# Kernel optimization log

Hardware: AMD Instinct MI355X
Metric: run time of the kernel (lower is better)

Reference implementation:

```python
import jax, jax.numpy as jnp
import numpy as np

N = 50000       # nodes
E = 800000      # edges (before self-loops)
F_IN = 128      # per-head input features (nfeat * t_size, t_size=1)
NHID = 128
NHEADS = 4
NCLASS = 64
NEG_SLOPE = 0.2   # GATConv leakyrelu negative_slope
ALPHA = 0.2       # outer LeakyReLU(alpha)


def setup_inputs():
    key = jax.random.key(0)
    ks = jax.random.split(key, 10)
    type_emb = jax.random.normal(ks[0], (NHEADS, N, F_IN), jnp.float32)
    edge = jax.random.randint(ks[1], (2, E), 0, N, dtype=jnp.int32)
    W = jax.random.normal(ks[2], (NHEADS, F_IN, NHID), jnp.float32) / np.sqrt(F_IN).astype(np.float32)
    att_src = jax.random.normal(ks[3], (NHEADS, NHID), jnp.float32) * 0.1
    att_dst = jax.random.normal(ks[4], (NHEADS, NHID), jnp.float32) * 0.1
    bias = jnp.zeros((NHEADS, NHID), jnp.float32)
    W_out = jax.random.normal(ks[5], (NHID * NHEADS, NCLASS), jnp.float32) / np.sqrt(NHID * NHEADS).astype(np.float32)
    att_src_out = jax.random.normal(ks[6], (NCLASS,), jnp.float32) * 0.1
    att_dst_out = jax.random.normal(ks[7], (NCLASS,), jnp.float32) * 0.1
    bias_out = jnp.zeros((NCLASS,), jnp.float32)
    return {"type_emb": type_emb, "edge": edge, "W": W, "att_src": att_src,
            "att_dst": att_dst, "bias": bias, "W_out": W_out,
            "att_src_out": att_src_out, "att_dst_out": att_dst_out,
            "bias_out": bias_out}


def _gat_conv(x, src, dst, W, a_src, a_dst, b):
    """PyG GATConv, heads=1, with self-loops already in (src, dst)."""
    xs = x @ W                                      # [N, H]
    e = jax.nn.leaky_relu((xs @ a_src)[src] + (xs @ a_dst)[dst], NEG_SLOPE)  # [E']
    # segment softmax over destination nodes (every node has a self-loop -> no empty segment)
    m = jax.ops.segment_max(e, dst, num_segments=N)
    ex = jnp.exp(e - m[dst])
    denom = jax.ops.segment_sum(ex, dst, num_segments=N)
    alpha = ex / denom[dst]                          # [E']
    out = jax.ops.segment_sum(alpha[:, None] * xs[src], dst, num_segments=N)  # [N, H]
    return out + b


def reference(type_emb, edge, W, att_src, att_dst, bias, W_out,
              att_src_out, att_dst_out, bias_out):
    loop = jnp.arange(N, dtype=edge.dtype)
    src = jnp.concatenate([edge[0], loop])
    dst = jnp.concatenate([edge[1], loop])
    # per-head GraphAttentionLayer: GATConv -> LeakyReLU(alpha) (dropout inactive)
    heads = [jax.nn.leaky_relu(
                 _gat_conv(type_emb[i], src, dst, W[i], att_src[i], att_dst[i], bias[i]),
                 ALPHA)
             for i in range(NHEADS)]
    x = jnp.concatenate(heads, axis=1)               # [N, NHID*NHEADS]
    y = jax.nn.leaky_relu(
            _gat_conv(x, src, dst, W_out, att_src_out, att_dst_out, bias_out),
            ALPHA)
    return jnp.tanh(y)                               # [N, NCLASS]
```

## Files before the change

kernel.cpp:

```cpp
#include <hip/hip_runtime.h>
#include <cmath>

#define NN 50000
#define EE 800000
#define ETOT (EE + NN)
#define NSCAN ((NN + 1023) / 1024)

typedef __bf16 v8bf __attribute__((ext_vector_type(8)));
typedef float f32x4 __attribute__((ext_vector_type(4)));

__device__ __forceinline__ float lrelu(float x){ return x > 0.0f ? x : 0.2f * x; }
__device__ __forceinline__ int bcast_i(int v, int j){ return __builtin_amdgcn_readlane(v, j); }
__device__ __forceinline__ float bcast_f(float v, int j){
  return __uint_as_float(__builtin_amdgcn_readlane(__float_as_uint(v), j));
}
__device__ __forceinline__ unsigned short f2bf_rne(float x){
  unsigned int u = __float_as_uint(x);
  u += 0x7fffu + ((u >> 16) & 1u);
  return (unsigned short)(u >> 16);
}
__device__ __forceinline__ float bf2f(unsigned short b){
  return __uint_as_float(((unsigned int)b) << 16);
}

__global__ void k_hist(const int* __restrict__ dst, int* __restrict__ cnt){
  int i = blockIdx.x * 256 + threadIdx.x;
  if (i >= ETOT) return;
  int d = (i < EE) ? dst[i] : (i - EE);
  atomicAdd(&cnt[d], 1);
}

__global__ void k_scan1(const int* __restrict__ cnt, int* __restrict__ part){
  __shared__ int sm[256];
  int b = blockIdx.x, t = threadIdx.x;
  int base = b * 1024 + t * 4;
  int s = 0;
  #pragma unroll
  for (int j = 0; j < 4; j++) if (base + j < NN) s += cnt[base + j];
  sm[t] = s; __syncthreads();
  for (int off = 128; off; off >>= 1){
    if (t < off) sm[t] += sm[t + off];
    __syncthreads();
  }
  if (t == 0) part[b] = sm[0];
}

__global__ void k_scan2(const int* __restrict__ part, int* __restrict__ part2){
  if (threadIdx.x == 0 && blockIdx.x == 0){
    int run = 0;
    for (int i = 0; i < NSCAN; i++){ part2[i] = run; run += part[i]; }
  }
}

__global__ void k_scan3(const int* __restrict__ cnt, const int* __restrict__ part2,
                        int* __restrict__ rowptr){
  __shared__ int sm[256];
  int b = blockIdx.x, t = threadIdx.x;
  int base = b * 1024 + t * 4;
  int v[4]; int s = 0;
  #pragma unroll
  for (int j = 0; j < 4; j++){ v[j] = (base + j < NN) ? cnt[base + j] : 0; s += v[j]; }
  sm[t] = s; __syncthreads();
  for (int off = 1; off < 256; off <<= 1){
    int x = (t >= off) ? sm[t - off] : 0;
    __syncthreads();
    sm[t] += x;
    __syncthreads();
  }
  int run = part2[b] + sm[t] - s;
  #pragma unroll
  for (int j = 0; j < 4; j++){
    if (base + j < NN){ rowptr[base + j] = run; run += v[j]; }
  }
  if (b == 0 && t == 0) rowptr[NN] = ETOT;
}

__global__ void k_scatter(const int* __restrict__ src, const int* __restrict__ dst,
                          const int* __restrict__ rowptr, int* __restrict__ fill,
                          int* __restrict__ csr){
  int i = blockIdx.x * 256 + threadIdx.x;
  if (i >= ETOT) return;
  int s, d;
  if (i < EE){ s = src[i]; d = dst[i]; } else { s = d = i - EE; }
  int pos = rowptr[d] + atomicAdd(&fill[d], 1);
  csr[pos] = s;
}

__global__ void k_convB(const float* __restrict__ B, unsigned short* __restrict__ bh,
                        unsigned short* __restrict__ bl, int K, int N, int total){
  int i = blockIdx.x * 256 + threadIdx.x;
  if (i >= total) return;
  int per = K * N;
  int h = i / per, rem = i - h * per;
  int k = rem / N, n = rem - k * N;
  float x = B[i];
  unsigned short hb = f2bf_rne(x);
  unsigned short lb = f2bf_rne(x - bf2f(hb));
  size_t o = (size_t)h * per + ((size_t)(k >> 3) * N + n) * 8 + (k & 7);
  bh[o] = hb; bl[o] = lb;
}

template<int BN, int OSTR>
__global__ __launch_bounds__(256) void gemm_split(const float* __restrict__ A,
                                                  const unsigned short* __restrict__ Bh,
                                                  const unsigned short* __restrict__ Bl,
                                                  unsigned short* __restrict__ out,
                                                  int M, int K){
  const int t = threadIdx.x;
  const int wv = t >> 6, lane = t & 63;
  const int m0 = blockIdx.x * 128;
  const int h = blockIdx.y;
  A  += (size_t)h * M * K;
  Bh += (size_t)h * (K >> 3) * BN * 8;
  Bl += (size_t)h * (K >> 3) * BN * 8;
  const int colOff = h * BN;

  __shared__ v8bf sAh[4][128];
  __shared__ v8bf sAl[4][128];
  __shared__ v8bf sBh[4][BN];
  __shared__ v8bf sBl[4][BN];

  f32x4 acc[2][BN / 16];
  #pragma unroll
  for (int i = 0; i < 2; i++)
    #pragma unroll
    for (int j = 0; j < BN / 16; j++){
      f32x4 z = {0.f, 0.f, 0.f, 0.f};
      acc[i][j] = z;
    }

  const int mRow = t & 127;
  const int kh = (t >> 7) * 16;
  const bool valid = (m0 + mRow) < M;
  const int q = lane >> 4, lm = lane & 15;

  for (int k0 = 0; k0 < K; k0 += 32){
    const float* ap = A + (size_t)(m0 + mRow) * K + k0 + kh;
    float4 v0, v1, v2, v3;
    if (valid){
      v0 = *(const float4*)(ap);
      v1 = *(const float4*)(ap + 4);
      v2 = *(const float4*)(ap + 8);
      v3 = *(const float4*)(ap + 12);
    } else {
      v0 = v1 = v2 = v3 = make_float4(0.f, 0.f, 0.f, 0.f);
    }
    #pragma unroll
    for (int g = 0; g < 2; g++){
      float xv[8];
      if (g == 0){ xv[0]=v0.x; xv[1]=v0.y; xv[2]=v0.z; xv[3]=v0.w; xv[4]=v1.x; xv[5]=v1.y; xv[6]=v1.z; xv[7]=v1.w; }
      else       { xv[0]=v2.x; xv[1]=v2.y; xv[2]=v2.z; xv[3]=v2.w; xv[4]=v3.x; xv[5]=v3.y; xv[6]=v3.z; xv[7]=v3.w; }
      union { v8bf v; unsigned short u[8]; } H, L;
      #pragma unroll
      for (int i = 0; i < 8; i++){
        unsigned short hb = f2bf_rne(xv[i]);
        H.u[i] = hb;
        L.u[i] = f2bf_rne(xv[i] - bf2f(hb));
      }
      int k8 = (kh >> 3) + g;
      sAh[k8][mRow] = H.v;
      sAl[k8][mRow] = L.v;
    }
    {
      const v8bf* gh = (const v8bf*)Bh + (size_t)(k0 >> 3) * BN;
      const v8bf* gl = (const v8bf*)Bl + (size_t)(k0 >> 3) * BN;
      v8bf* dh = &sBh[0][0];
      v8bf* dl = &sBl[0][0];
      #pragma unroll
      for (int i = t; i < 4 * BN; i += 256){ dh[i] = gh[i]; dl[i] = gl[i]; }
    }
    __syncthreads();
    v8bf ah[2], al[2];
    #pragma unroll
    for (int rt = 0; rt < 2; rt++){
      int m = wv * 32 + rt * 16 + lm;
      ah[rt] = sAh[q][m];
      al[rt] = sAl[q][m];
    }
    #pragma unroll
    for (int ct = 0; ct < BN / 16; ct++){
      v8bf bh = sBh[q][ct * 16 + lm];
      v8bf bl = sBl[q][ct * 16 + lm];
      #pragma unroll
      for (int rt = 0; rt < 2; rt++){
        acc[rt][ct] = __builtin_amdgcn_mfma_f32_16x16x32_bf16(ah[rt], bh, acc[rt][ct], 0, 0, 0);
        acc[rt][ct] = __builtin_amdgcn_mfma_f32_16x16x32_bf16(ah[rt], bl, acc[rt][ct], 0, 0, 0);
        acc[rt][ct] = __builtin_amdgcn_mfma_f32_16x16x32_bf16(al[rt], bh, acc[rt][ct], 0, 0, 0);
      }
    }
    __syncthreads();
  }

  #pragma unroll
  for (int rt = 0; rt < 2; rt++){
    #pragma unroll
    for (int reg = 0; reg < 4; reg++){
      int r = m0 + wv * 32 + rt * 16 + q * 4 + reg;
      if (r < M){
        unsigned short* orow = out + (size_t)r * OSTR + colOff + lm;
        #pragma unroll
        for (int ct = 0; ct < BN / 16; ct++)
          orow[ct * 16] = f2bf_rne(acc[rt][ct][reg]);
      }
    }
  }
}

__global__ __launch_bounds__(256) void k_rowdot_all(const unsigned short* __restrict__ xs_all,
                                                    const float* __restrict__ att_src,
                                                    const float* __restrict__ att_dst,
                                                    float* __restrict__ ssrc,
                                                    float* __restrict__ sdst){
  int n = (blockIdx.x * 256 + threadIdx.x) >> 6;
  int lane = threadIdx.x & 63;
  if (n >= NN) return;
  int h = lane >> 4, c8 = lane & 15;
  uint4 u = ((const uint4*)xs_all)[(size_t)n * 64 + lane];
  const float* as = att_src + h * 128 + c8 * 8;
  const float* ad = att_dst + h * 128 + c8 * 8;
  float4 a0 = *(const float4*)as, a1 = *(const float4*)(as + 4);
  float4 b0 = *(const float4*)ad, b1 = *(const float4*)(ad + 4);
  float f[8];
  f[0] = __uint_as_float(u.x << 16); f[1] = __uint_as_float(u.x & 0xffff0000u);
  f[2] = __uint_as_float(u.y << 16); f[3] = __uint_as_float(u.y & 0xffff0000u);
  f[4] = __uint_as_float(u.z << 16); f[5] = __uint_as_float(u.z & 0xffff0000u);
  f[6] = __uint_as_float(u.w << 16); f[7] = __uint_as_float(u.w & 0xffff0000u);
  float d0 = f[0]*a0.x + f[1]*a0.y + f[2]*a0.z + f[3]*a0.w
           + f[4]*a1.x + f[5]*a1.y + f[6]*a1.z + f[7]*a1.w;
  float d1 = f[0]*b0.x + f[1]*b0.y + f[2]*b0.z + f[3]*b0.w
           + f[4]*b1.x + f[5]*b1.y + f[6]*b1.z + f[7]*b1.w;
  #pragma unroll
  for (int off = 1; off < 16; off <<= 1){
    d0 += __shfl_xor(d0, off, 64);
    d1 += __shfl_xor(d1, off, 64);
  }
  if (c8 == 0){ ssrc[n * 4 + h] = d0; sdst[n * 4 + h] = d1; }
}

__global__ __launch_bounds__(256) void k_agg4(const int* __restrict__ rowptr,
                                              const int* __restrict__ csr,
                                              const float* __restrict__ ssrc,
                                              const float* __restrict__ sdst,
                                              const unsigned short* __restrict__ xs_all,
                                              const float* __restrict__ bias,
                                              float* __restrict__ x1){
  int n = (blockIdx.x * 256 + threadIdx.x) >> 6;
  int lane = threadIdx.x & 63;
  if (n >= NN) return;
  int start = rowptr[n], end = rowptr[n + 1];
  float4 sd = ((const float4*)sdst)[n];

  float m0 = -3.0e38f, m1 = -3.0e38f, m2 = -3.0e38f, m3 = -3.0e38f;
  for (int e = start + lane; e < end; e += 64){
    float4 sv = ((const float4*)ssrc)[csr[e]];
    m0 = fmaxf(m0, lrelu(sv.x + sd.x));
    m1 = fmaxf(m1, lrelu(sv.y + sd.y));
    m2 = fmaxf(m2, lrelu(sv.z + sd.z));
    m3 = fmaxf(m3, lrelu(sv.w + sd.w));
  }
  #pragma unroll
  for (int off = 32; off; off >>= 1){
    m0 = fmaxf(m0, __shfl_xor(m0, off, 64));
    m1 = fmaxf(m1, __shfl_xor(m1, off, 64));
    m2 = fmaxf(m2, __shfl_xor(m2, off, 64));
    m3 = fmaxf(m3, __shfl_xor(m3, off, 64));
  }

  float s0 = 0.f, s1 = 0.f, s2 = 0.f, s3 = 0.f;
  for (int e = start + lane; e < end; e += 64){
    float4 sv = ((const float4*)ssrc)[csr[e]];
    s0 += __expf(lrelu(sv.x + sd.x) - m0);
    s1 += __expf(lrelu(sv.y + sd.y) - m1);
    s2 += __expf(lrelu(sv.z + sd.z) - m2);
    s3 += __expf(lrelu(sv.w + sd.w) - m3);
  }
  #pragma unroll
  for (int off = 32; off; off >>= 1){
    s0 += __shfl_xor(s0, off, 64);
    s1 += __shfl_xor(s1, off, 64);
    s2 += __shfl_xor(s2, off, 64);
    s3 += __shfl_xor(s3, off, 64);
  }
  float i0 = 1.f / s0, i1 = 1.f / s1, i2 = 1.f / s2, i3 = 1.f / s3;

  int myh = lane >> 4;
  float acc[8];
  #pragma unroll
  for (int i = 0; i < 8; i++) acc[i] = 0.f;
  for (int cb = start; cb < end; cb += 64){
    int e = cb + lane;
    int sl = 0; float w0 = 0.f, w1 = 0.f, w2 = 0.f, w3 = 0.f;
    if (e < end){
      sl = csr[e];
      float4 sv = ((const float4*)ssrc)[sl];
      w0 = __expf(lrelu(sv.x + sd.x) - m0) * i0;
      w1 = __expf(lrelu(sv.y + sd.y) - m1) * i1;
      w2 = __expf(lrelu(sv.z + sd.z) - m2) * i2;
      w3 = __expf(lrelu(sv.w + sd.w) - m3) * i3;
    }
    int cnt = min(64, end - cb);
    for (int j = 0; j < cnt; j++){
      int s = bcast_i(sl, j);
      float wa = bcast_f(w0, j), wb = bcast_f(w1, j);
      float wc = bcast_f(w2, j), wd = bcast_f(w3, j);
      float wm = (myh == 0) ? wa : (myh == 1) ? wb : (myh == 2) ? wc : wd;
      uint4 u = ((const uint4*)xs_all)[(size_t)s * 64 + lane];
      acc[0] += wm * __uint_as_float(u.x << 16);
      acc[1] += wm * __uint_as_float(u.x & 0xffff0000u);
      acc[2] += wm * __uint_as_float(u.y << 16);
      acc[3] += wm * __uint_as_float(u.y & 0xffff0000u);
      acc[4] += wm * __uint_as_float(u.z << 16);
      acc[5] += wm * __uint_as_float(u.z & 0xffff0000u);
      acc[6] += wm * __uint_as_float(u.w << 16);
      acc[7] += wm * __uint_as_float(u.w & 0xffff0000u);
    }
  }

  const float* bp = bias + lane * 8;
  float4 bb0 = *(const float4*)bp, bb1 = *(const float4*)(bp + 4);
  float o[8];
  o[0] = lrelu(acc[0] + bb0.x); o[1] = lrelu(acc[1] + bb0.y);
  o[2] = lrelu(acc[2] + bb0.z); o[3] = lrelu(acc[3] + bb0.w);
  o[4] = lrelu(acc[4] + bb1.x); o[5] = lrelu(acc[5] + bb1.y);
  o[6] = lrelu(acc[6] + bb1.z); o[7] = lrelu(acc[7] + bb1.w);
  float* op = x1 + (size_t)n * 512 + lane * 8;
  *(float4*)op       = make_float4(o[0], o[1], o[2], o[3]);
  *(float4*)(op + 4) = make_float4(o[4], o[5], o[6], o[7]);
}

__global__ __launch_bounds__(256) void k_rowdot2(const unsigned short* __restrict__ xs2,
                                                 const float* __restrict__ as,
                                                 const float* __restrict__ ad,
                                                 float* __restrict__ ssrc,
                                                 float* __restrict__ sdst){
  int idx = blockIdx.x * 256 + threadIdx.x;
  int n = idx >> 5, sub = idx & 31;
  if (n >= NN) return;
  unsigned int u = ((const unsigned int*)xs2)[n * 32 + sub];
  float f0 = __uint_as_float(u << 16);
  float f1 = __uint_as_float(u & 0xffff0000u);
  float d0 = f0 * as[sub * 2] + f1 * as[sub * 2 + 1];
  float d1 = f0 * ad[sub * 2] + f1 * ad[sub * 2 + 1];
  #pragma unroll
  for (int off = 1; off < 32; off <<= 1){
    d0 += __shfl_xor(d0, off, 64);
    d1 += __shfl_xor(d1, off, 64);
  }
  if (sub == 0){ ssrc[n] = d0; sdst[n] = d1; }
}

__global__ __launch_bounds__(256) void k_agg2(const int* __restrict__ rowptr,
                                              const int* __restrict__ csr,
                                              const float* __restrict__ ssrc,
                                              const float* __restrict__ sdst,
                                              const unsigned short* __restrict__ xs2,
                                              const float* __restrict__ bias,
                                              float* __restrict__ outp){
  int n = (blockIdx.x * 256 + threadIdx.x) >> 6;
  int lane = threadIdx.x & 63;
  if (n >= NN) return;
  int start = rowptr[n], end = rowptr[n + 1];
  float sdn = sdst[n];

  float mloc = -3.0e38f;
  for (int e = start + lane; e < end; e += 64)
    mloc = fmaxf(mloc, lrelu(ssrc[csr[e]] + sdn));
  #pragma unroll
  for (int off = 32; off; off >>= 1) mloc = fmaxf(mloc, __shfl_xor(mloc, off, 64));

  float sloc = 0.f;
  for (int e = start + lane; e < end; e += 64)
    sloc += __expf(lrelu(ssrc[csr[e]] + sdn) - mloc);
  #pragma unroll
  for (int off = 32; off; off >>= 1) sloc += __shfl_xor(sloc, off, 64);
  float inv = 1.f / sloc;

  int half = lane >> 5, sub = lane & 31;
  float acc0 = 0.f, acc1 = 0.f;
  for (int cb = start; cb < end; cb += 64){
    int e = cb + lane;
    int sl = 0; float w = 0.f;
    if (e < end){
      sl = csr[e];
      w = __expf(lrelu(ssrc[sl] + sdn) - mloc) * inv;
    }
    int cnt = min(64, end - cb);
    for (int jj = 0; jj * 2 < cnt; jj++){
      int j0 = jj * 2, j1 = jj * 2 + 1;
      int sa = bcast_i(sl, j0); float wa = bcast_f(w, j0);
      int sb = bcast_i(sl, j1); float wb = bcast_f(w, j1);
      int ss = half ? sb : sa;
      float ws = half ? wb : wa;
      unsigned int u = ((const unsigned int*)xs2)[(size_t)ss * 32 + sub];
      acc0 += ws * __uint_as_float(u << 16);
      acc1 += ws * __uint_as_float(u & 0xffff0000u);
    }
  }
  acc0 += __shfl_xor(acc0, 32, 64);
  acc1 += __shfl_xor(acc1, 32, 64);
  if (lane < 32){
    float o0 = tanhf(lrelu(acc0 + bias[sub * 2]));
    float o1 = tanhf(lrelu(acc1 + bias[sub * 2 + 1]));
    *(float2*)(outp + (size_t)n * 64 + sub * 2) = make_float2(o0, o1);
  }
}

extern "C" void kernel_launch(void* const* d_in, const int* in_sizes, int n_in,
                              void* d_out, int out_size, void* d_ws, size_t ws_size,
                              hipStream_t stream){
  const float* type_emb  = (const float*)d_in[0];
  const int*   edge      = (const int*)d_in[1];
  const float* W         = (const float*)d_in[2];
  const float* att_src   = (const float*)d_in[3];
  const float* att_dst   = (const float*)d_in[4];
  const float* bias      = (const float*)d_in[5];
  const float* W_out     = (const float*)d_in[6];
  const float* att_src_o = (const float*)d_in[7];
  const float* att_dst_o = (const float*)d_in[8];
  const float* bias_o    = (const float*)d_in[9];
  float* out = (float*)d_out;
  (void)in_sizes; (void)n_in; (void)out_size; (void)ws_size;

  char* ws = (char*)d_ws;
  size_t off = 0;
  auto alloc = [&](size_t bytes) -> void* {
    void* p = ws + off;
    off = (off + bytes + 255) & ~(size_t)255;
    return p;
  };
  unsigned short* xs_all = (unsigned short*)alloc((size_t)NN * 512 * 2);
  float*          x1     = (float*)alloc((size_t)NN * 512 * 4);
  unsigned short* xs2    = (unsigned short*)alloc((size_t)NN * 64 * 2);
  float* ssrc1 = (float*)alloc((size_t)NN * 4 * 4);
  float* sdst1 = (float*)alloc((size_t)NN * 4 * 4);
  float* ssrc2 = (float*)alloc((size_t)NN * 4);
  float* sdst2 = (float*)alloc((size_t)NN * 4);
  int* cnt    = (int*)alloc((size_t)NN * 4);
  int* rowptr = (int*)alloc((size_t)(NN + 1) * 4);
  int* fill   = (int*)alloc((size_t)NN * 4);
  int* csr    = (int*)alloc((size_t)ETOT * 4);
  int* p1     = (int*)alloc((size_t)NSCAN * 4 + 256);
  int* p2     = (int*)alloc((size_t)NSCAN * 4 + 256);
  unsigned short* Bh1 = (unsigned short*)alloc((size_t)4 * 128 * 128 * 2);
  unsigned short* Bl1 = (unsigned short*)alloc((size_t)4 * 128 * 128 * 2);
  unsigned short* Bh2 = (unsigned short*)alloc((size_t)512 * 64 * 2);
  unsigned short* Bl2 = (unsigned short*)alloc((size_t)512 * 64 * 2);

  hipMemsetAsync(cnt, 0, (size_t)NN * 4, stream);
  hipMemsetAsync(fill, 0, (size_t)NN * 4, stream);
  k_hist<<<(ETOT + 255) / 256, 256, 0, stream>>>(edge + EE, cnt);
  k_scan1<<<NSCAN, 256, 0, stream>>>(cnt, p1);
  k_scan2<<<1, 64, 0, stream>>>(p1, p2);
  k_scan3<<<NSCAN, 256, 0, stream>>>(cnt, p2, rowptr);
  k_scatter<<<(ETOT + 255) / 256, 256, 0, stream>>>(edge, edge + EE, rowptr, fill, csr);

  k_convB<<<(4 * 128 * 128 + 255) / 256, 256, 0, stream>>>(W, Bh1, Bl1, 128, 128, 4 * 128 * 128);
  k_convB<<<(512 * 64 + 255) / 256, 256, 0, stream>>>(W_out, Bh2, Bl2, 512, 64, 512 * 64);

  gemm_split<128, 512><<<dim3(391, 4), 256, 0, stream>>>(type_emb, Bh1, Bl1, xs_all, NN, 128);
  k_rowdot_all<<<12500, 256, 0, stream>>>(xs_all, att_src, att_dst, ssrc1, sdst1);
  k_agg4<<<12500, 256, 0, stream>>>(rowptr, csr, ssrc1, sdst1, xs_all, bias, x1);

  gemm_split<64, 64><<<dim3(391, 1), 256, 0, stream>>>(x1, Bh2, Bl2, xs2, NN, 512);
  k_rowdot2<<<(NN * 32 + 255) / 256, 256, 0, stream>>>(xs2, att_src_o, att_dst_o, ssrc2, sdst2);
  k_agg2<<<12500, 256, 0, stream>>>(rowptr, csr, ssrc2, sdst2, xs2, bias_o, out);
}
```

Measured before the change: 518.0 us.

## Slice feature matrices by 32 columns and split aggregation into weight and gather passes

GEMM outputs are now stored column-sliced, in 32-column slabs laid out node-major, so each aggregation pass gathers from a compact 64-byte-per-node slice that fits the cache better. Softmax edge weights are computed once into per-edge buffers, and separate gather kernels then aggregate per slice, with blocks ordered so the 8 slices of a phase run together. This cuts the random-gather working set per phase, at the cost of extra edge-weight buffers written to and re-read from memory, reading csr once per slice, and many more blocks to launch.

New measurement: 725.6 us. 1.4x slower.

```diff
diff --git a/kernel.cpp b/kernel.cpp
--- a/kernel.cpp
+++ b/kernel.cpp
@@ -10,10 +10,6 @@
 typedef float f32x4 __attribute__((ext_vector_type(4)));
 
 __device__ __forceinline__ float lrelu(float x){ return x > 0.0f ? x : 0.2f * x; }
-__device__ __forceinline__ int bcast_i(int v, int j){ return __builtin_amdgcn_readlane(v, j); }
-__device__ __forceinline__ float bcast_f(float v, int j){
-  return __uint_as_float(__builtin_amdgcn_readlane(__float_as_uint(v), j));
-}
 __device__ __forceinline__ unsigned short f2bf_rne(float x){
   unsigned int u = __float_as_uint(x);
   u += 0x7fffu + ((u >> 16) & 1u);
@@ -100,7 +96,7 @@
   bh[o] = hb; bl[o] = lb;
 }
 
-template<int BN, int OSTR>
+template<int BN>
 __global__ __launch_bounds__(256) void gemm_split(const float* __restrict__ A,
                                                   const unsigned short* __restrict__ Bh,
                                                   const unsigned short* __restrict__ Bl,
@@ -197,16 +193,17 @@
     for (int reg = 0; reg < 4; reg++){
       int r = m0 + wv * 32 + rt * 16 + q * 4 + reg;
       if (r < M){
-        unsigned short* orow = out + (size_t)r * OSTR + colOff + lm;
         #pragma unroll
-        for (int ct = 0; ct < BN / 16; ct++)
-          orow[ct * 16] = f2bf_rne(acc[rt][ct][reg]);
+        for (int ct = 0; ct < BN / 16; ct++){
+          int col = colOff + ct * 16 + lm;
+          out[((size_t)(col >> 5) * NN + r) * 32 + (col & 31)] = f2bf_rne(acc[rt][ct][reg]);
+        }
       }
     }
   }
 }
 
-__global__ __launch_bounds__(256) void k_rowdot_all(const unsigned short* __restrict__ xs_all,
+__global__ __launch_bounds__(256) void k_rowdot_all(const unsigned short* __restrict__ xs_sl,
                                                     const float* __restrict__ att_src,
                                                     const float* __restrict__ att_dst,
                                                     float* __restrict__ ssrc,
@@ -215,9 +212,9 @@
   int lane = threadIdx.x & 63;
   if (n >= NN) return;
   int h = lane >> 4, c8 = lane & 15;
-  uint4 u = ((const uint4*)xs_all)[(size_t)n * 64 + lane];
-  const float* as = att_src + h * 128 + c8 * 8;
-  const float* ad = att_dst + h * 128 + c8 * 8;
+  uint4 u = ((const uint4*)xs_sl)[((size_t)(lane >> 2) * NN + n) * 4 + (lane & 3)];
+  const float* as = att_src + lane * 8;
+  const float* ad = att_dst + lane * 8;
   float4 a0 = *(const float4*)as, a1 = *(const float4*)(as + 4);
   float4 b0 = *(const float4*)ad, b1 = *(const float4*)(ad + 4);
   float f[8];
@@ -237,13 +234,11 @@
   if (c8 == 0){ ssrc[n * 4 + h] = d0; sdst[n * 4 + h] = d1; }
 }
 
-__global__ __launch_bounds__(256) void k_agg4(const int* __restrict__ rowptr,
-                                              const int* __restrict__ csr,
-                                              const float* __restrict__ ssrc,
-                                              const float* __restrict__ sdst,
-                                              const unsigned short* __restrict__ xs_all,
-                                              const float* __restrict__ bias,
-                                              float* __restrict__ x1){
+__global__ __launch_bounds__(256) void k_weights4(const int* __restrict__ rowptr,
+                                                  const int* __restrict__ csr,
+                                                  const float* __restrict__ ssrc,
+                                                  const float* __restrict__ sdst,
+                                                  float* __restrict__ w4){
   int n = (blockIdx.x * 256 + threadIdx.x) >> 6;
   int lane = threadIdx.x & 63;
   if (n >= NN) return;
@@ -283,52 +278,67 @@
   }
   float i0 = 1.f / s0, i1 = 1.f / s1, i2 = 1.f / s2, i3 = 1.f / s3;
 
-  int myh = lane >> 4;
-  float acc[8];
-  #pragma unroll
-  for (int i = 0; i < 8; i++) acc[i] = 0.f;
-  for (int cb = start; cb < end; cb += 64){
-    int e = cb + lane;
-    int sl = 0; float w0 = 0.f, w1 = 0.f, w2 = 0.f, w3 = 0.f;
+  for (int e = start + lane; e < end; e += 64){
+    float4 sv = ((const float4*)ssrc)[csr[e]];
+    float4 w;
+    w.x = __expf(lrelu(sv.x + sd.x) - m0) * i0;
+    w.y = __expf(lrelu(sv.y + sd.y) - m1) * i1;
+    w.z = __expf(lrelu(sv.z + sd.z) - m2) * i2;
+    w.w = __expf(lrelu(sv.w + sd.w) - m3) * i3;
+    ((float4*)w4)[e] = w;
+  }
+}
+
+__global__ __launch_bounds__(256) void k_gagg1(const int* __restrict__ rowptr,
+                                               const int* __restrict__ csr,
+                                               const float* __restrict__ w4,
+                                               const unsigned short* __restrict__ xs_sl,
+                                               const float* __restrict__ bias,
+                                               float* __restrict__ x1){
+  int b = blockIdx.x;
+  int phase = b / (8 * 12500);
+  int rem = b - phase * 8 * 12500;
+  int chunk = rem >> 3, slo = rem & 7;
+  int slice = phase * 8 + slo;
+  int wv = threadIdx.x >> 6, lane = threadIdx.x & 63;
+  int n = chunk * 4 + wv;
+  int start = rowptr[n], end = rowptr[n + 1];
+  int g = lane >> 3, l = lane & 7;
+  int h = slice >> 2;
+  const unsigned short* xb = xs_sl + (size_t)slice * NN * 32;
+  float a0 = 0.f, a1 = 0.f, a2 = 0.f, a3 = 0.f;
+  for (int cb = start; cb < end; cb += 8){
+    int e = cb + g;
     if (e < end){
-      sl = csr[e];
-      float4 sv = ((const float4*)ssrc)[sl];
-      w0 = __expf(lrelu(sv.x + sd.x) - m0) * i0;
-      w1 = __expf(lrelu(sv.y + sd.y) - m1) * i1;
-      w2 = __expf(lrelu(sv.z + sd.z) - m2) * i2;
-      w3 = __expf(lrelu(sv.w + sd.w) - m3) * i3;
-    }
-    int cnt = min(64, end - cb);
-    for (int j = 0; j < cnt; j++){
-      int s = bcast_i(sl, j);
-      float wa = bcast_f(w0, j), wb = bcast_f(w1, j);
-      float wc = bcast_f(w2, j), wd = bcast_f(w3, j);
-      float wm = (myh == 0) ? wa : (myh == 1) ? wb : (myh == 2) ? wc : wd;
-      uint4 u = ((const uint4*)xs_all)[(size_t)s * 64 + lane];
-      acc[0] += wm * __uint_as_float(u.x << 16);
-      acc[1] += wm * __uint_as_float(u.x & 0xffff0000u);
-      acc[2] += wm * __uint_as_float(u.y << 16);
-      acc[3] += wm * __uint_as_float(u.y & 0xffff0000u);
-      acc[4] += wm * __uint_as_float(u.z << 16);
-      acc[5] += wm * __uint_as_float(u.z & 0xffff0000u);
-      acc[6] += wm * __uint_as_float(u.w << 16);
-      acc[7] += wm * __uint_as_float(u.w & 0xffff0000u);
-    }
-  }
-
-  const float* bp = bias + lane * 8;
-  float4 bb0 = *(const float4*)bp, bb1 = *(const float4*)(bp + 4);
-  float o[8];
-  o[0] = lrelu(acc[0] + bb0.x); o[1] = lrelu(acc[1] + bb0.y);
-  o[2] = lrelu(acc[2] + bb0.z); o[3] = lrelu(acc[3] + bb0.w);
-  o[4] = lrelu(acc[4] + bb1.x); o[5] = lrelu(acc[5] + bb1.y);
-  o[6] = lrelu(acc[6] + bb1.z); o[7] = lrelu(acc[7] + bb1.w);
-  float* op = x1 + (size_t)n * 512 + lane * 8;
-  *(float4*)op       = make_float4(o[0], o[1], o[2], o[3]);
-  *(float4*)(op + 4) = make_float4(o[4], o[5], o[6], o[7]);
-}
-
-__global__ __launch_bounds__(256) void k_rowdot2(const unsigned short* __restrict__ xs2,
+      int s = csr[e];
+      float w = w4[e * 4 + h];
+      uint2 u = *(const uint2*)(xb + (size_t)s * 32 + l * 4);
+      a0 += w * __uint_as_float(u.x << 16);
+      a1 += w * __uint_as_float(u.x & 0xffff0000u);
+      a2 += w * __uint_as_float(u.y << 16);
+      a3 += w * __uint_as_float(u.y & 0xffff0000u);
+    }
+  }
+  #pragma unroll
+  for (int off = 8; off < 64; off <<= 1){
+    a0 += __shfl_xor(a0, off, 64);
+    a1 += __shfl_xor(a1, off, 64);
+    a2 += __shfl_xor(a2, off, 64);
+    a3 += __shfl_xor(a3, off, 64);
+  }
+  if (g == 0){
+    const float* bp = bias + slice * 32 + l * 4;
+    float4 bb = *(const float4*)bp;
+    float4 o;
+    o.x = lrelu(a0 + bb.x);
+    o.y = lrelu(a1 + bb.y);
+    o.z = lrelu(a2 + bb.z);
+    o.w = lrelu(a3 + bb.w);
+    *(float4*)(x1 + (size_t)n * 512 + slice * 32 + l * 4) = o;
+  }
+}
+
+__global__ __launch_bounds__(256) void k_rowdot2(const unsigned short* __restrict__ xs2_sl,
                                                  const float* __restrict__ as,
                                                  const float* __restrict__ ad,
                                                  float* __restrict__ ssrc,
@@ -336,7 +346,7 @@
   int idx = blockIdx.x * 256 + threadIdx.x;
   int n = idx >> 5, sub = idx & 31;
   if (n >= NN) return;
-  unsigned int u = ((const unsigned int*)xs2)[n * 32 + sub];
+  unsigned int u = ((const unsigned int*)xs2_sl)[((size_t)(sub >> 4) * NN + n) * 16 + (sub & 15)];
   float f0 = __uint_as_float(u << 16);
   float f1 = __uint_as_float(u & 0xffff0000u);
   float d0 = f0 * as[sub * 2] + f1 * as[sub * 2 + 1];
@@ -349,13 +359,11 @@
   if (sub == 0){ ssrc[n] = d0; sdst[n] = d1; }
 }
 
-__global__ __launch_bounds__(256) void k_agg2(const int* __restrict__ rowptr,
-                                              const int* __restrict__ csr,
-                                              const float* __restrict__ ssrc,
-                                              const float* __restrict__ sdst,
-                                              const unsigned short* __restrict__ xs2,
-                                              const float* __restrict__ bias,
-                                              float* __restrict__ outp){
+__global__ __launch_bounds__(256) void k_weights1(const int* __restrict__ rowptr,
+                                                  const int* __restrict__ csr,
+                                                  const float* __restrict__ ssrc,
+                                                  const float* __restrict__ sdst,
+                                                  float* __restrict__ w2){
   int n = (blockIdx.x * 256 + threadIdx.x) >> 6;
   int lane = threadIdx.x & 63;
   if (n >= NN) return;
@@ -375,33 +383,54 @@
   for (int off = 32; off; off >>= 1) sloc += __shfl_xor(sloc, off, 64);
   float inv = 1.f / sloc;
 
-  int half = lane >> 5, sub = lane & 31;
-  float acc0 = 0.f, acc1 = 0.f;
-  for (int cb = start; cb < end; cb += 64){
-    int e = cb + lane;
-    int sl = 0; float w = 0.f;
+  for (int e = start + lane; e < end; e += 64)
+    w2[e] = __expf(lrelu(ssrc[csr[e]] + sdn) - mloc) * inv;
+}
+
+__global__ __launch_bounds__(256) void k_gagg2(const int* __restrict__ rowptr,
+                                               const int* __restrict__ csr,
+                                               const float* __restrict__ w2,
+                                               const unsigned short* __restrict__ xs2_sl,
+                                               const float* __restrict__ bias,
+                                               float* __restrict__ outp){
+  int b = blockIdx.x;
+  int chunk = b >> 3, t = b & 7;
+  int slice = t >> 2, sub = t & 3;
+  int wv = threadIdx.x >> 6, lane = threadIdx.x & 63;
+  int n = chunk * 16 + sub * 4 + wv;
+  if (n >= NN) return;
+  int start = rowptr[n], end = rowptr[n + 1];
+  int g = lane >> 3, l = lane & 7;
+  const unsigned short* xb = xs2_sl + (size_t)slice * NN * 32;
+  float a0 = 0.f, a1 = 0.f, a2 = 0.f, a3 = 0.f;
+  for (int cb = start; cb < end; cb += 8){
+    int e = cb + g;
     if (e < end){
-      sl = csr[e];
-      w = __expf(lrelu(ssrc[sl] + sdn) - mloc) * inv;
-    }
-    int cnt = min(64, end - cb);
-    for (int jj = 0; jj * 2 < cnt; jj++){
-      int j0 = jj * 2, j1 = jj * 2 + 1;
-      int sa = bcast_i(sl, j0); float wa = bcast_f(w, j0);
-      int sb = bcast_i(sl, j1); float wb = bcast_f(w, j1);
-      int ss = half ? sb : sa;
-      float ws = half ? wb : wa;
-      unsigned int u = ((const unsigned int*)xs2)[(size_t)ss * 32 + sub];
-      acc0 += ws * __uint_as_float(u << 16);
-      acc1 += ws * __uint_as_float(u & 0xffff0000u);
-    }
-  }
-  acc0 += __shfl_xor(acc0, 32, 64);
-  acc1 += __shfl_xor(acc1, 32, 64);
-  if (lane < 32){
-    float o0 = tanhf(lrelu(acc0 + bias[sub * 2]));
-    float o1 = tanhf(lrelu(acc1 + bias[sub * 2 + 1]));
-    *(float2*)(outp + (size_t)n * 64 + sub * 2) = make_float2(o0, o1);
+      int s = csr[e];
+      float w = w2[e];
+      uint2 u = *(const uint2*)(xb + (size_t)s * 32 + l * 4);
+      a0 += w * __uint_as_float(u.x << 16);
+      a1 += w * __uint_as_float(u.x & 0xffff0000u);
+      a2 += w * __uint_as_float(u.y << 16);
+      a3 += w * __uint_as_float(u.y & 0xffff0000u);
+    }
+  }
+  #pragma unroll
+  for (int off = 8; off < 64; off <<= 1){
+    a0 += __shfl_xor(a0, off, 64);
+    a1 += __shfl_xor(a1, off, 64);
+    a2 += __shfl_xor(a2, off, 64);
+    a3 += __shfl_xor(a3, off, 64);
+  }
+  if (g == 0){
+    const float* bp = bias + slice * 32 + l * 4;
+    float4 bb = *(const float4*)bp;
+    float4 o;
+    o.x = tanhf(lrelu(a0 + bb.x));
+    o.y = tanhf(lrelu(a1 + bb.y));
+    o.z = tanhf(lrelu(a2 + bb.z));
+    o.w = tanhf(lrelu(a3 + bb.w));
+    *(float4*)(outp + (size_t)n * 64 + slice * 32 + l * 4) = o;
   }
 }
 
@@ -428,9 +457,11 @@
     off = (off + bytes + 255) & ~(size_t)255;
     return p;
   };
-  unsigned short* xs_all = (unsigned short*)alloc((size_t)NN * 512 * 2);
+  unsigned short* xs_sl1 = (unsigned short*)alloc((size_t)NN * 512 * 2);
   float*          x1     = (float*)alloc((size_t)NN * 512 * 4);
-  unsigned short* xs2    = (unsigned short*)alloc((size_t)NN * 64 * 2);
+  unsigned short* xs2_sl = (unsigned short*)alloc((size_t)NN * 64 * 2);
+  float* w4    = (float*)alloc((size_t)ETOT * 4 * 4);
+  float* w2    = (float*)alloc((size_t)ETOT * 4);
   float* ssrc1 = (float*)alloc((size_t)NN * 4 * 4);
   float* sdst1 = (float*)alloc((size_t)NN * 4 * 4);
   float* ssrc2 = (float*)alloc((size_t)NN * 4);
@@ -457,11 +488,13 @@
   k_convB<<<(4 * 128 * 128 + 255) / 256, 256, 0, stream>>>(W, Bh1, Bl1, 128, 128, 4 * 128 * 128);
   k_convB<<<(512 * 64 + 255) / 256, 256, 0, stream>>>(W_out, Bh2, Bl2, 512, 64, 512 * 64);
 
-  gemm_split<128, 512><<<dim3(391, 4), 256, 0, stream>>>(type_emb, Bh1, Bl1, xs_all, NN, 128);
-  k_rowdot_all<<<12500, 256, 0, stream>>>(xs_all, att_src, att_dst, ssrc1, sdst1);
-  k_agg4<<<12500, 256, 0, stream>>>(rowptr, csr, ssrc1, sdst1, xs_all, bias, x1);
-
-  gemm_split<64, 64><<<dim3(391, 1), 256, 0, stream>>>(x1, Bh2, Bl2, xs2, NN, 512);
-  k_rowdot2<<<(NN * 32 + 255) / 256, 256, 0, stream>>>(xs2, att_src_o, att_dst_o, ssrc2, sdst2);
-  k_agg2<<<12500, 256, 0, stream>>>(rowptr, csr, ssrc2, sdst2, xs2, bias_o, out);
-}
+  gemm_split<128><<<dim3(391, 4), 256, 0, stream>>>(type_emb, Bh1, Bl1, xs_sl1, NN, 128);
+  k_rowdot_all<<<12500, 256, 0, stream>>>(xs_sl1, att_src, att_dst, ssrc1, sdst1);
+  k_weights4<<<12500, 256, 0, stream>>>(rowptr, csr, ssrc1, sdst1, w4);
+  k_gagg1<<<200000, 256, 0, stream>>>(rowptr, csr, w4, xs_sl1, bias, x1);
+
+  gemm_split<64><<<dim3(391, 1), 256, 0, stream>>>(x1, Bh2, Bl2, xs2_sl, NN, 512);
+  k_rowdot2<<<(NN * 32 + 255) / 256, 256, 0, stream>>>(xs2_sl, att_src_o, att_dst_o, ssrc2, sdst2);
+  k_weights1<<<12500, 256, 0, stream>>>(rowptr, csr, ssrc2, sdst2, w2);
+  k_gagg2<<<25000, 256, 0, stream>>>(rowptr, csr, w2, xs2_sl, bias_o, out);
+}
```

## Split GAT aggregation into edge-weight and gather kernels, drop softmax max pass

Applied to the files above, without the earlier changes.

Each aggregation kernel is split in two. The first computes unnormalized exp edge weights without max subtraction, stores them per edge, and saves the inverse sums. The second gathers neighbour features using the stored weights and applies the normalization at the end. The change removes the max pass and the repeated recomputation of scores, and packs the accumulation into float2 vectors. In exchange it adds an extra launch and edge-weight traffic to memory, and risks exp overflow without the max shift.

Measured after the change: 533.4 us. +3.0%, slower.

```diff
diff --git a/kernel.cpp b/kernel.cpp
--- a/kernel.cpp
+++ b/kernel.cpp
@@ -8,6 +8,7 @@
 
 typedef __bf16 v8bf __attribute__((ext_vector_type(8)));
 typedef float f32x4 __attribute__((ext_vector_type(4)));
+typedef float f32x2 __attribute__((ext_vector_type(2)));
 
 __device__ __forceinline__ float lrelu(float x){ return x > 0.0f ? x : 0.2f * x; }
 __device__ __forceinline__ int bcast_i(int v, int j){ return __builtin_amdgcn_readlane(v, j); }
@@ -216,8 +217,8 @@
   if (n >= NN) return;
   int h = lane >> 4, c8 = lane & 15;
   uint4 u = ((const uint4*)xs_all)[(size_t)n * 64 + lane];
-  const float* as = att_src + h * 128 + c8 * 8;
-  const float* ad = att_dst + h * 128 + c8 * 8;
+  const float* as = att_src + lane * 8;
+  const float* ad = att_dst + lane * 8;
   float4 a0 = *(const float4*)as, a1 = *(const float4*)(as + 4);
   float4 b0 = *(const float4*)ad, b1 = *(const float4*)(ad + 4);
   float f[8];
@@ -237,42 +238,28 @@
   if (c8 == 0){ ssrc[n * 4 + h] = d0; sdst[n * 4 + h] = d1; }
 }
 
-__global__ __launch_bounds__(256) void k_agg4(const int* __restrict__ rowptr,
-                                              const int* __restrict__ csr,
-                                              const float* __restrict__ ssrc,
-                                              const float* __restrict__ sdst,
-                                              const unsigned short* __restrict__ xs_all,
-                                              const float* __restrict__ bias,
-                                              float* __restrict__ x1){
+__global__ __launch_bounds__(256) void k_weights4(const int* __restrict__ rowptr,
+                                                  const int* __restrict__ csr,
+                                                  const float* __restrict__ ssrc,
+                                                  const float* __restrict__ sdst,
+                                                  float* __restrict__ w4,
+                                                  float* __restrict__ inv4){
   int n = (blockIdx.x * 256 + threadIdx.x) >> 6;
   int lane = threadIdx.x & 63;
   if (n >= NN) return;
   int start = rowptr[n], end = rowptr[n + 1];
   float4 sd = ((const float4*)sdst)[n];
-
-  float m0 = -3.0e38f, m1 = -3.0e38f, m2 = -3.0e38f, m3 = -3.0e38f;
-  for (int e = start + lane; e < end; e += 64){
-    float4 sv = ((const float4*)ssrc)[csr[e]];
-    m0 = fmaxf(m0, lrelu(sv.x + sd.x));
-    m1 = fmaxf(m1, lrelu(sv.y + sd.y));
-    m2 = fmaxf(m2, lrelu(sv.z + sd.z));
-    m3 = fmaxf(m3, lrelu(sv.w + sd.w));
-  }
-  #pragma unroll
-  for (int off = 32; off; off >>= 1){
-    m0 = fmaxf(m0, __shfl_xor(m0, off, 64));
-    m1 = fmaxf(m1, __shfl_xor(m1, off, 64));
-    m2 = fmaxf(m2, __shfl_xor(m2, off, 64));
-    m3 = fmaxf(m3, __shfl_xor(m3, off, 64));
-  }
 
   float s0 = 0.f, s1 = 0.f, s2 = 0.f, s3 = 0.f;
   for (int e = start + lane; e < end; e += 64){
     float4 sv = ((const float4*)ssrc)[csr[e]];
-    s0 += __expf(lrelu(sv.x + sd.x) - m0);
-    s1 += __expf(lrelu(sv.y + sd.y) - m1);
-    s2 += __expf(lrelu(sv.z + sd.z) - m2);
-    s3 += __expf(lrelu(sv.w + sd.w) - m3);
+    float4 w;
+    w.x = __expf(lrelu(sv.x + sd.x));
+    w.y = __expf(lrelu(sv.y + sd.y));
+    w.z = __expf(lrelu(sv.z + sd.z));
+    w.w = __expf(lrelu(sv.w + sd.w));
+    ((float4*)w4)[e] = w;
+    s0 += w.x; s1 += w.y; s2 += w.z; s3 += w.w;
   }
   #pragma unroll
   for (int off = 32; off; off >>= 1){
@@ -281,22 +268,34 @@
     s2 += __shfl_xor(s2, off, 64);
     s3 += __shfl_xor(s3, off, 64);
   }
-  float i0 = 1.f / s0, i1 = 1.f / s1, i2 = 1.f / s2, i3 = 1.f / s3;
-
+  if (lane == 0){
+    float4 iv;
+    iv.x = 1.f / s0; iv.y = 1.f / s1; iv.z = 1.f / s2; iv.w = 1.f / s3;
+    ((float4*)inv4)[n] = iv;
+  }
+}
+
+__global__ __launch_bounds__(256) void k_gagg4(const int* __restrict__ rowptr,
+                                               const int* __restrict__ csr,
+                                               const float* __restrict__ w4,
+                                               const float* __restrict__ inv4,
+                                               const unsigned short* __restrict__ xs_all,
+                                               const float* __restrict__ bias,
+                                               float* __restrict__ x1){
+  int n = (blockIdx.x * 256 + threadIdx.x) >> 6;
+  int lane = threadIdx.x & 63;
+  if (n >= NN) return;
+  int start = rowptr[n], end = rowptr[n + 1];
   int myh = lane >> 4;
-  float acc[8];
-  #pragma unroll
-  for (int i = 0; i < 8; i++) acc[i] = 0.f;
+
+  f32x2 a01 = {0.f, 0.f}, a23 = {0.f, 0.f}, a45 = {0.f, 0.f}, a67 = {0.f, 0.f};
   for (int cb = start; cb < end; cb += 64){
     int e = cb + lane;
     int sl = 0; float w0 = 0.f, w1 = 0.f, w2 = 0.f, w3 = 0.f;
     if (e < end){
       sl = csr[e];
-      float4 sv = ((const float4*)ssrc)[sl];
-      w0 = __expf(lrelu(sv.x + sd.x) - m0) * i0;
-      w1 = __expf(lrelu(sv.y + sd.y) - m1) * i1;
-      w2 = __expf(lrelu(sv.z + sd.z) - m2) * i2;
-      w3 = __expf(lrelu(sv.w + sd.w) - m3) * i3;
+      float4 wv = ((const float4*)w4)[e];
+      w0 = wv.x; w1 = wv.y; w2 = wv.z; w3 = wv.w;
     }
     int cnt = min(64, end - cb);
     for (int j = 0; j < cnt; j++){
@@ -304,25 +303,29 @@
       float wa = bcast_f(w0, j), wb = bcast_f(w1, j);
       float wc = bcast_f(w2, j), wd = bcast_f(w3, j);
       float wm = (myh == 0) ? wa : (myh == 1) ? wb : (myh == 2) ? wc : wd;
+      f32x2 wv2 = {wm, wm};
       uint4 u = ((const uint4*)xs_all)[(size_t)s * 64 + lane];
-      acc[0] += wm * __uint_as_float(u.x << 16);
-      acc[1] += wm * __uint_as_float(u.x & 0xffff0000u);
-      acc[2] += wm * __uint_as_float(u.y << 16);
-      acc[3] += wm * __uint_as_float(u.y & 0xffff0000u);
-      acc[4] += wm * __uint_as_float(u.z << 16);
-      acc[5] += wm * __uint_as_float(u.z & 0xffff0000u);
-      acc[6] += wm * __uint_as_float(u.w << 16);
-      acc[7] += wm * __uint_as_float(u.w & 0xffff0000u);
-    }
-  }
-
+      f32x2 v;
+      v.x = __uint_as_float(u.x << 16); v.y = __uint_as_float(u.x & 0xffff0000u);
+      a01 += wv2 * v;
+      v.x = __uint_as_float(u.y << 16); v.y = __uint_as_float(u.y & 0xffff0000u);
+      a23 += wv2 * v;
+      v.x = __uint_as_float(u.z << 16); v.y = __uint_as_float(u.z & 0xffff0000u);
+      a45 += wv2 * v;
+      v.x = __uint_as_float(u.w << 16); v.y = __uint_as_float(u.w & 0xffff0000u);
+      a67 += wv2 * v;
+    }
+  }
+
+  float4 iv = ((const float4*)inv4)[n];
+  float inv = (myh == 0) ? iv.x : (myh == 1) ? iv.y : (myh == 2) ? iv.z : iv.w;
   const float* bp = bias + lane * 8;
   float4 bb0 = *(const float4*)bp, bb1 = *(const float4*)(bp + 4);
   float o[8];
-  o[0] = lrelu(acc[0] + bb0.x); o[1] = lrelu(acc[1] + bb0.y);
-  o[2] = lrelu(acc[2] + bb0.z); o[3] = lrelu(acc[3] + bb0.w);
-  o[4] = lrelu(acc[4] + bb1.x); o[5] = lrelu(acc[5] + bb1.y);
-  o[6] = lrelu(acc[6] + bb1.z); o[7] = lrelu(acc[7] + bb1.w);
+  o[0] = lrelu(a01.x * inv + bb0.x); o[1] = lrelu(a01.y * inv + bb0.y);
+  o[2] = lrelu(a23.x * inv + bb0.z); o[3] = lrelu(a23.y * inv + bb0.w);
+  o[4] = lrelu(a45.x * inv + bb1.x); o[5] = lrelu(a45.y * inv + bb1.y);
+  o[6] = lrelu(a67.x * inv + bb1.z); o[7] = lrelu(a67.y * inv + bb1.w);
   float* op = x1 + (size_t)n * 512 + lane * 8;
   *(float4*)op       = make_float4(o[0], o[1], o[2], o[3]);
   *(float4*)(op + 4) = make_float4(o[4], o[5], o[6], o[7]);
@@ -349,40 +352,49 @@
   if (sub == 0){ ssrc[n] = d0; sdst[n] = d1; }
 }
 
-__global__ __launch_bounds__(256) void k_agg2(const int* __restrict__ rowptr,
-                                              const int* __restrict__ csr,
-                                              const float* __restrict__ ssrc,
-                                              const float* __restrict__ sdst,
-                                              const unsigned short* __restrict__ xs2,
-                                              const float* __restrict__ bias,
-                                              float* __restrict__ outp){
+__global__ __launch_bounds__(256) void k_weights1(const int* __restrict__ rowptr,
+                                                  const int* __restrict__ csr,
+                                                  const float* __restrict__ ssrc,
+                                                  const float* __restrict__ sdst,
+                                                  float* __restrict__ w2,
+                                                  float* __restrict__ inv2){
   int n = (blockIdx.x * 256 + threadIdx.x) >> 6;
   int lane = threadIdx.x & 63;
   if (n >= NN) return;
   int start = rowptr[n], end = rowptr[n + 1];
   float sdn = sdst[n];
 
-  float mloc = -3.0e38f;
-  for (int e = start + lane; e < end; e += 64)
-    mloc = fmaxf(mloc, lrelu(ssrc[csr[e]] + sdn));
-  #pragma unroll
-  for (int off = 32; off; off >>= 1) mloc = fmaxf(mloc, __shfl_xor(mloc, off, 64));
-
   float sloc = 0.f;
-  for (int e = start + lane; e < end; e += 64)
-    sloc += __expf(lrelu(ssrc[csr[e]] + sdn) - mloc);
+  for (int e = start + lane; e < end; e += 64){
+    float w = __expf(lrelu(ssrc[csr[e]] + sdn));
+    w2[e] = w;
+    sloc += w;
+  }
   #pragma unroll
   for (int off = 32; off; off >>= 1) sloc += __shfl_xor(sloc, off, 64);
-  float inv = 1.f / sloc;
-
+  if (lane == 0) inv2[n] = 1.f / sloc;
+}
+
+__global__ __launch_bounds__(256) void k_gagg2(const int* __restrict__ rowptr,
+                                               const int* __restrict__ csr,
+                                               const float* __restrict__ w2,
+                                               const float* __restrict__ inv2,
+                                               const unsigned short* __restrict__ xs2,
+                                               const float* __restrict__ bias,
+                                               float* __restrict__ outp){
+  int n = (blockIdx.x * 256 + threadIdx.x) >> 6;
+  int lane = threadIdx.x & 63;
+  if (n >= NN) return;
+  int start = rowptr[n], end = rowptr[n + 1];
   int half = lane >> 5, sub = lane & 31;
-  float acc0 = 0.f, acc1 = 0.f;
+
+  f32x2 acc = {0.f, 0.f};
   for (int cb = start; cb < end; cb += 64){
     int e = cb + lane;
     int sl = 0; float w = 0.f;
     if (e < end){
       sl = csr[e];
-      w = __expf(lrelu(ssrc[sl] + sdn) - mloc) * inv;
+      w = w2[e];
     }
     int cnt = min(64, end - cb);
     for (int jj = 0; jj * 2 < cnt; jj++){
@@ -392,15 +404,19 @@
       int ss = half ? sb : sa;
       float ws = half ? wb : wa;
       unsigned int u = ((const unsigned int*)xs2)[(size_t)ss * 32 + sub];
-      acc0 += ws * __uint_as_float(u << 16);
-      acc1 += ws * __uint_as_float(u & 0xffff0000u);
-    }
-  }
-  acc0 += __shfl_xor(acc0, 32, 64);
-  acc1 += __shfl_xor(acc1, 32, 64);
+      f32x2 wv2 = {ws, ws};
+      f32x2 v;
+      v.x = __uint_as_float(u << 16);
+      v.y = __uint_as_float(u & 0xffff0000u);
+      acc += wv2 * v;
+    }
+  }
+  acc.x += __shfl_xor(acc.x, 32, 64);
+  acc.y += __shfl_xor(acc.y, 32, 64);
   if (lane < 32){
-    float o0 = tanhf(lrelu(acc0 + bias[sub * 2]));
-    float o1 = tanhf(lrelu(acc1 + bias[sub * 2 + 1]));
+    float inv = inv2[n];
+    float o0 = tanhf(lrelu(acc.x * inv + bias[sub * 2]));
+    float o1 = tanhf(lrelu(acc.y * inv + bias[sub * 2 + 1]));
     *(float2*)(outp + (size_t)n * 64 + sub * 2) = make_float2(o0, o1);
   }
 }
@@ -431,6 +447,10 @@
   unsigned short* xs_all = (unsigned short*)alloc((size_t)NN * 512 * 2);
   float*          x1     = (float*)alloc((size_t)NN * 512 * 4);
   unsigned short* xs2    = (unsigned short*)alloc((size_t)NN * 64 * 2);
+  float* w4    = (float*)alloc((size_t)ETOT * 4 * 4);
+  float* w2    = (float*)alloc((size_t)ETOT * 4);
+  float* inv4  = (float*)alloc((size_t)NN * 4 * 4);
+  float* inv2  = (float*)alloc((size_t)NN * 4);
   float* ssrc1 = (float*)alloc((size_t)NN * 4 * 4);
   float* sdst1 = (float*)alloc((size_t)NN * 4 * 4);
   float* ssrc2 = (float*)alloc((size_t)NN * 4);
@@ -459,9 +479,11 @@
 
   gemm_split<128, 512><<<dim3(391, 4), 256, 0, stream>>>(type_emb, Bh1, Bl1, xs_all, NN, 128);
   k_rowdot_all<<<12500, 256, 0, stream>>>(xs_all, att_src, att_dst, ssrc1, sdst1);
-  k_agg4<<<12500, 256, 0, stream>>>(rowptr, csr, ssrc1, sdst1, xs_all, bias, x1);
+  k_weights4<<<12500, 256, 0, stream>>>(rowptr, csr, ssrc1, sdst1, w4, inv4);
+  k_gagg4<<<12500, 256, 0, stream>>>(rowptr, csr, w4, inv4, xs_all, bias, x1);
 
   gemm_split<64, 64><<<dim3(391, 1), 256, 0, stream>>>(x1, Bh2, Bl2, xs2, NN, 512);
   k_rowdot2<<<(NN * 32 + 255) / 256, 256, 0, stream>>>(xs2, att_src_o, att_dst_o, ssrc2, sdst2);
-  k_agg2<<<12500, 256, 0, stream>>>(rowptr, csr, ssrc2, sdst2, xs2, bias_o, out);
-}
+  k_weights1<<<12500, 256, 0, stream>>>(rowptr, csr, ssrc2, sdst2, w2, inv2);
+  k_gagg2<<<12500, 256, 0, stream>>>(rowptr, csr, w2, inv2, xs2, bias_o, out);
+}
```
